# Kernel optimization log

Hardware: AMD Instinct MI355X
Metric: run time of the kernel (lower is better)

## Reference

```python
import jax, jax.numpy as jnp
import numpy as np

N, E, DIN, D, FE, L, B, M = 10000, 40000, 11, 64, 4, 4, 512, 3


def setup_inputs() -> dict:
    key = jax.random.key(0)
    ks = iter(jax.random.split(key, 24))
    s = lambda *sh: jax.random.normal(next(ks), sh, jnp.float32)
    return {
        "x": s(N, DIN),
        "edge_index": jax.random.randint(next(ks), (2, E), 0, N),
        "edge_attr": jax.random.uniform(next(ks), (E, FE), jnp.float32),
        "batch": jnp.sort(jax.random.randint(next(ks), (N,), 0, B)),
        "W0": s(DIN, D) * 0.1, "b0": jnp.zeros((D,), jnp.float32),
        "Wn1": s(FE, 2 * D) * 0.1, "bn1": jnp.zeros((2 * D,), jnp.float32),
        "Wn2": s(2 * D, D * D) * 0.02, "bn2": jnp.zeros((D * D,), jnp.float32),
        "root": s(L, D, D) * 0.1, "conv_bias": jnp.zeros((L, D), jnp.float32),
        "lstm_Wih": s(4 * D, 2 * D) * 0.1, "lstm_Whh": s(4 * D, D) * 0.1,
        "lstm_b": jnp.zeros((4 * D,), jnp.float32),
        "Wo1": s(2 * D, D) * 0.1, "bo1": jnp.zeros((D,), jnp.float32),
        "Wo2": s(D, 1) * 0.1, "bo2": jnp.zeros((1,), jnp.float32),
    }


def reference(x, edge_index, edge_attr, batch, W0, b0, Wn1, bn1, Wn2, bn2,
              root, conv_bias, lstm_Wih, lstm_Whh, lstm_b, Wo1, bo1, Wo2, bo2):
    src, dst = edge_index[0], edge_index[1]
    h = x @ W0 + b0  # [N, D]
    # Edge MLP is SHARED across all conv layers -> compute per-edge weight matrices once
    ew = (jax.nn.silu(edge_attr @ Wn1 + bn1) @ Wn2 + bn2).reshape(E, D, D)
    for l in range(L):
        msg = jnp.einsum('ed,edf->ef', h[src], ew)  # gather-compute per edge
        aggr = jax.ops.segment_sum(msg, dst, num_segments=N)  # scatter-add to targets
        h = h + (aggr + h @ root[l] + conv_bias[l])  # NNConv + residual
    # Set2Set pooling (LSTM, M processing steps)
    q_star = jnp.zeros((B, 2 * D), h.dtype)
    hs = jnp.zeros((B, D), h.dtype)
    cs = jnp.zeros((B, D), h.dtype)
    for _ in range(M):
        gates = q_star @ lstm_Wih.T + hs @ lstm_Whh.T + lstm_b
        i, f, g, o = jnp.split(gates, 4, axis=-1)  # torch LSTM gate order
        cs = jax.nn.sigmoid(f) * cs + jax.nn.sigmoid(i) * jnp.tanh(g)
        hs = jax.nn.sigmoid(o) * jnp.tanh(cs)
        q = hs  # [B, D]
        e = jnp.sum(h * q[batch], axis=-1)  # [N]
        emax = jax.ops.segment_max(e, batch, num_segments=B)
        ex = jnp.exp(e - emax[batch])
        denom = jax.ops.segment_sum(ex, batch, num_segments=B)
        a = ex / denom[batch]  # per-graph softmax attention
        r = jax.ops.segment_sum(a[:, None] * h, batch, num_segments=B)
        q_star = jnp.concatenate([q, r], axis=-1)
    out = jax.nn.silu(q_star @ Wo1 + bo1) @ Wo2 + bo2
    return out.reshape(-1)
```

## Files before the change

kernel.cpp:

```cpp
#include <hip/hip_runtime.h>
#include <cstdint>
#include <cstddef>

#define NN   10000
#define EE   40000
#define DIN_ 11
#define DD   64
#define LL   4
#define BB   512
#define MM   3
#define K1   128
#define DD2  4096
#define NPB  16
#define NCH  8
#define CSPL 2
#define CPB  4
#define ESLOT 12
#define ECREG (8 * ESLOT)
#define EHW (ECREG * 8)

typedef unsigned short ushort_t;
typedef unsigned int   uint_t;

typedef __bf16 bf16x8_t __attribute__((ext_vector_type(8)));
typedef float  f32x4_t  __attribute__((ext_vector_type(4)));
union FragU { uint4 u; bf16x8_t b; };

__device__ __forceinline__ float bfu(ushort_t u) { return __uint_as_float(((uint_t)u) << 16); }
__device__ __forceinline__ float bflo(uint_t u) { return __uint_as_float(u << 16); }
__device__ __forceinline__ float bfhi(uint_t u) { return __uint_as_float(u & 0xffff0000u); }
__device__ __forceinline__ ushort_t f2bf(float f) {
  uint_t u = __float_as_uint(f);
  u = (u + 0x7fffu + ((u >> 16) & 1u)) >> 16;
  return (ushort_t)u;
}
__device__ __forceinline__ uint_t pack2(float lo, float hi) {
  return (uint_t)f2bf(lo) | ((uint_t)f2bf(hi) << 16);
}
__device__ __forceinline__ float sigmf_(float x) { return 1.f / (1.f + expf(-x)); }
__device__ __forceinline__ float siluf_(float x) { return x / (1.f + expf(-x)); }

#if defined(__HIP_DEVICE_COMPILE__) && __has_builtin(__builtin_amdgcn_fdot2_f32_bf16)
typedef __bf16 bf16x2_t __attribute__((ext_vector_type(2)));
__device__ __forceinline__ float dot2a(uint_t a, uint_t b, float c) {
  union { uint_t u; bf16x2_t v; } ua, ub;
  ua.u = a; ub.u = b;
  return __builtin_amdgcn_fdot2_f32_bf16(ua.v, ub.v, c, false);
}
#else
__device__ __forceinline__ float dot2a(uint_t a, uint_t b, float c) {
  return c + bflo(a) * bflo(b) + bfhi(a) * bfhi(b);
}
#endif

#define NCANON 16
struct CanonArgs {
  const void* src[NCANON];
  float* dst[NCANON];
  int n[NCANON];
};
__global__ void k_canon(CanonArgs a, const ushort_t* __restrict__ ea, int* __restrict__ flag) {
  __shared__ int bad;
  if (threadIdx.x == 0) bad = 0;
  __syncthreads();
  ushort_t u = ea[threadIdx.x];
  if ((u & 0x8000u) || u > 0x3F80u) atomicAdd(&bad, 1);
  __syncthreads();
  const int isbf = (bad == 0) ? 1 : 0;
  if (blockIdx.x == 0 && blockIdx.y == 0 && threadIdx.x == 0) *flag = isbf;
  const int ai = blockIdx.y;
  const int n = a.n[ai];
  const int i = blockIdx.x * 256 + threadIdx.x;
  if (i >= n) return;
  float v;
  if (isbf) v = bfu(((const ushort_t*)a.src[ai])[i]);
  else      v = ((const float*)a.src[ai])[i];
  a.dst[ai][i] = v;
}

__global__ void k_wn2m(const void* __restrict__ Wn2, uint_t* __restrict__ out,
                       const int* __restrict__ flag) {
  __shared__ ushort_t row[DD2];
  const int k = blockIdx.x, tid = threadIdx.x;
  if (*flag) {
    const uint4* src = (const uint4*)((const ushort_t*)Wn2 + (size_t)k * DD2);
    ((uint4*)row)[tid] = src[tid];
    ((uint4*)row)[tid + 256] = src[tid + 256];
  } else {
    const float* src = (const float*)Wn2 + (size_t)k * DD2;
    for (int j = 0; j < 16; ++j) row[tid + 256 * j] = f2bf(src[tid + 256 * j]);
  }
  __syncthreads();
  const int kpg = k >> 1, par = k & 1;
  const int lane = tid >> 2, jp = tid & 3;
  const int q = lane >> 4, n = lane & 15;
  for (int fc = 0; fc < 4; ++fc) {
#pragma unroll
    for (int hf = 0; hf < 2; ++hf) {
      int d0 = hf * 32 + q * 8 + 2 * jp;
      int f = fc * 16 + n;
      uint_t lo = row[d0 * 64 + f], hi = row[(d0 + 1) * 64 + f];
      out[((((size_t)kpg * 4 + fc) * 2 + par) * 2 + hf) * 256 + tid] = lo | (hi << 16);
    }
  }
}

__global__ void k_wT(const float* __restrict__ Wihc, const float* __restrict__ Whhc,
                     float* __restrict__ Wiht, float* __restrict__ Whht) {
  int idx = blockIdx.x * 256 + threadIdx.x;
  if (idx < 4 * DD * K1) {
    int j = idx >> 7, i = idx & 127;
    Wiht[i * 256 + j] = Wihc[idx];
  }
  if (idx < 4 * DD * DD) {
    int j = idx >> 6, i = idx & 63;
    Whht[i * 256 + j] = Whhc[idx];
  }
}

__global__ void k_embed(const float* __restrict__ x, const float* __restrict__ W0,
                        const float* __restrict__ b0, const float* __restrict__ bn2,
                        float* __restrict__ h, uint_t* __restrict__ hpk,
                        float* __restrict__ nbias) {
  __shared__ float xs[DIN_];
  __shared__ float hl[DD];
  const int n = blockIdx.x, f = threadIdx.x;
  if (f < DIN_) xs[f] = x[n * DIN_ + f];
  __syncthreads();
  float a = b0[f];
  for (int i = 0; i < DIN_; ++i) a += xs[i] * W0[i * DD + f];
  h[(size_t)n * DD + f] = a;
  hl[f] = a;
  float other = __shfl_down(a, 1);
  if ((f & 1) == 0)
    hpk[(size_t)n * 32 + (f >> 1)] = pack2(a, other);
  __syncthreads();
  float nb = 0.f;
#pragma unroll
  for (int d = 0; d < DD; ++d) nb += hl[d] * bn2[d * DD + f];
  nbias[(size_t)n * DD + f] = nb;
}

__global__ void k_edgemlp(const float* __restrict__ ea, const float* __restrict__ Wn1,
                          const float* __restrict__ bn1, const int* __restrict__ epos,
                          uint_t* __restrict__ hn1c) {
  int idx = blockIdx.x * 256 + threadIdx.x;
  if (idx >= EE * (K1 / 2)) return;
  int e = idx >> 6, j = idx & 63;
  int k0 = 2 * j, k1 = 2 * j + 1;
  float a0 = ea[e * 4 + 0], a1 = ea[e * 4 + 1], a2 = ea[e * 4 + 2], a3 = ea[e * 4 + 3];
  float t0 = bn1[k0] + a0 * Wn1[k0] + a1 * Wn1[K1 + k0] + a2 * Wn1[2 * K1 + k0] + a3 * Wn1[3 * K1 + k0];
  float t1 = bn1[k1] + a0 * Wn1[k1] + a1 * Wn1[K1 + k1] + a2 * Wn1[2 * K1 + k1] + a3 * Wn1[3 * K1 + k1];
  int pos = epos[e];
  hn1c[((size_t)(j >> 3) * EE + pos) * 8 + (j & 7)] = pack2(siluf_(t0), siluf_(t1));
}

__global__ void k_hist(const int* __restrict__ ei, int* __restrict__ cnt_s) {
  int e = blockIdx.x * 256 + threadIdx.x;
  if (e >= EE) return;
  atomicAdd(&cnt_s[ei[e]], 1);
}

__global__ void k_scan(const int* __restrict__ cnt, int* __restrict__ rp,
                       const int* __restrict__ batch, int* __restrict__ goff) {
  if (blockIdx.x == 1) {
    int g = threadIdx.x;
    if (g > BB) return;
    int lo = 0, hi = NN;
    while (lo < hi) {
      int mid = (lo + hi) >> 1;
      if (batch[mid] < g) lo = mid + 1; else hi = mid;
    }
    goff[g] = lo;
    return;
  }
  __shared__ int part[1024];
  const int tid = threadIdx.x;
  const int chunk = (NN + 1023) / 1024;
  int s = 0;
  for (int j = 0; j < chunk; ++j) {
    int idx = tid * chunk + j;
    if (idx < NN) s += cnt[idx];
  }
  part[tid] = s;
  __syncthreads();
  for (int off = 1; off < 1024; off <<= 1) {
    int v = (tid >= off) ? part[tid - off] : 0;
    __syncthreads();
    part[tid] += v;
    __syncthreads();
  }
  int base = (tid == 0) ? 0 : part[tid - 1];
  for (int j = 0; j < chunk; ++j) {
    int idx = tid * chunk + j;
    if (idx < NN) { rp[idx] = base; base += cnt[idx]; }
  }
  if (tid == 1023) rp[NN] = part[1023];
}

__global__ void k_fill(const int* __restrict__ ei, const int* __restrict__ rps,
                       int* __restrict__ cur_s, int* __restrict__ epos,
                       int* __restrict__ esd) {
  int e = blockIdx.x * 256 + threadIdx.x;
  if (e >= EE) return;
  int s = ei[e], d = ei[EE + e];
  int ps = atomicAdd(&cur_s[s], 1);
  int pos = rps[s] + ps;
  epos[e] = pos;
  esd[2 * pos] = s;
  esd[2 * pos + 1] = d;
}

__global__ __launch_bounds__(512, 4) void k_conv(
    const uint_t* __restrict__ hpk, const uint_t* __restrict__ hn1c,
    const uint_t* __restrict__ Wn2m, const float* __restrict__ nbias,
    const int* __restrict__ rps, const int* __restrict__ esd,
    float* __restrict__ aggr) {
  __shared__ __align__(16) uint_t Gp[NPB * 2 * 64 * 4];
  __shared__ __align__(16) uint_t eh[CPB * EHW];
  __shared__ int2 eStage[ECREG];
  const int tid = threadIdx.x;
  const int w = tid >> 6, lane = tid & 63;
  const int q = lane >> 4, n16 = lane & 15;
  const int half = blockIdx.x / 625;
  const int ng = blockIdx.x - half * 625;
  const int n0 = ng * NPB;
  const int e0 = rps[n0], e1 = rps[n0 + NPB];
  const int ecnt = e1 - e0;
  const int ecap = ecnt < ECREG ? ecnt : ECREG;

  if (tid < ECREG && tid < ecnt) eStage[tid] = ((const int2*)esd)[e0 + tid];

  uint4 st0, st1, st2, st3;
  const bool stv = (tid < ecap * 2);
  if (stv) {
    const size_t base = ((size_t)(half * CPB) * EE + e0) * 8;
    st0 = ((const uint4*)(hn1c + base))[tid];
    st1 = ((const uint4*)(hn1c + base + (size_t)EE * 8))[tid];
    st2 = ((const uint4*)(hn1c + base + (size_t)2 * EE * 8))[tid];
    st3 = ((const uint4*)(hn1c + base + (size_t)3 * EE * 8))[tid];
  }

  FragU a0, a1;
  {
    const uint4* ap = (const uint4*)(hpk + (size_t)(n0 + n16) * 32);
    a0.u = ap[q];
    a1.u = ap[4 + q];
  }
  __syncthreads();

  float acc[ESLOT];
#pragma unroll
  for (int s = 0; s < ESLOT; ++s) {
    const int li = w + 8 * s;
    float v = 0.f;
    if (half == 0 && li < ecap)
      v = nbias[(size_t)eStage[li].x * 64 + lane];
    acc[s] = v;
  }

  if (stv) {
    ((uint4*)(eh + 0 * EHW))[tid] = st0;
    ((uint4*)(eh + 1 * EHW))[tid] = st1;
    ((uint4*)(eh + 2 * EHW))[tid] = st2;
    ((uint4*)(eh + 3 * EHW))[tid] = st3;
  }

  const int kq = w >> 2, fcw = w & 3;
  for (int cc = 0; cc < CPB; ++cc) {
    const int c = half * CPB + cc;
    if (cc) __syncthreads();
    uint_t pk[4][4];
#pragma unroll
    for (int slot = 0; slot < 4; ++slot) {
      const int kpg = c * 8 + kq * 4 + slot;
      const uint4* bp = (const uint4*)Wn2m + (size_t)(kpg * 4 + fcw) * 256 + lane;
      FragU b00, b01, b10, b11;
      b00.u = bp[0];
      b01.u = bp[64];
      b10.u = bp[128];
      b11.u = bp[192];
      f32x4_t acc0 = {0.f, 0.f, 0.f, 0.f};
      f32x4_t acc1 = {0.f, 0.f, 0.f, 0.f};
      acc0 = __builtin_amdgcn_mfma_f32_16x16x32_bf16(a0.b, b00.b, acc0, 0, 0, 0);
      acc0 = __builtin_amdgcn_mfma_f32_16x16x32_bf16(a1.b, b01.b, acc0, 0, 0, 0);
      acc1 = __builtin_amdgcn_mfma_f32_16x16x32_bf16(a0.b, b10.b, acc1, 0, 0, 0);
      acc1 = __builtin_amdgcn_mfma_f32_16x16x32_bf16(a1.b, b11.b, acc1, 0, 0, 0);
#pragma unroll
      for (int r = 0; r < 4; ++r) pk[r][slot] = pack2(acc0[r], acc1[r]);
    }
#pragma unroll
    for (int r = 0; r < 4; ++r) {
      const int m = q * 4 + r;
      uint4 v;
      v.x = pk[r][0]; v.y = pk[r][1]; v.z = pk[r][2]; v.w = pk[r][3];
      ((uint4*)Gp)[(size_t)(m * 2 + kq) * 64 + fcw * 16 + n16] = v;
    }
    __syncthreads();
    const uint4* ehb = (const uint4*)(eh + cc * EHW);
#pragma unroll
    for (int s = 0; s < ESLOT; ++s) {
      const int li = w + 8 * s;
      if (li < ecap) {
        const int2 sd = eStage[li];
        const int m = sd.x - n0;
        uint4 hv0 = ehb[li * 2], hv1 = ehb[li * 2 + 1];
        const uint4* gb = (const uint4*)Gp + (size_t)(m * 2) * 64 + lane;
        uint4 g0 = gb[0], g1 = gb[64];
        float p = acc[s];
        p = dot2a(g0.x, hv0.x, p);
        p = dot2a(g0.y, hv0.y, p);
        p = dot2a(g0.z, hv0.z, p);
        p = dot2a(g0.w, hv0.w, p);
        p = dot2a(g1.x, hv1.x, p);
        p = dot2a(g1.y, hv1.y, p);
        p = dot2a(g1.z, hv1.z, p);
        p = dot2a(g1.w, hv1.w, p);
        acc[s] = p;
      }
    }
    for (int li = ECREG + w; li < ecnt; li += 8) {
      const int ii = e0 + li;
      const int src = __builtin_amdgcn_readfirstlane(esd[2 * ii]);
      const int dst = __builtin_amdgcn_readfirstlane(esd[2 * ii + 1]);
      const int m = src - n0;
      float p = (half == 0 && cc == 0) ? nbias[(size_t)src * 64 + lane] : 0.f;
      const uint4* hp = (const uint4*)(hn1c + ((size_t)c * EE + ii) * 8);
      uint4 hv0 = hp[0], hv1 = hp[1];
      const uint4* gb = (const uint4*)Gp + (size_t)(m * 2) * 64 + lane;
      uint4 g0 = gb[0], g1 = gb[64];
      p = dot2a(g0.x, hv0.x, p);
      p = dot2a(g0.y, hv0.y, p);
      p = dot2a(g0.z, hv0.z, p);
      p = dot2a(g0.w, hv0.w, p);
      p = dot2a(g1.x, hv1.x, p);
      p = dot2a(g1.y, hv1.y, p);
      p = dot2a(g1.z, hv1.z, p);
      p = dot2a(g1.w, hv1.w, p);
      atomicAdd(&aggr[(size_t)dst * 64 + lane], p);
    }
  }
#pragma unroll
  for (int s = 0; s < ESLOT; ++s) {
    const int li = w + 8 * s;
    if (li < ecap) {
      const int dst = eStage[li].y;
      atomicAdd(&aggr[(size_t)dst * 64 + lane], acc[s]);
    }
  }
}

__global__ __launch_bounds__(256) void k_update(
    float* __restrict__ h, uint_t* __restrict__ hpk,
    float* __restrict__ aggr, const float* __restrict__ bn2,
    const float* __restrict__ root, const float* __restrict__ cb,
    float* __restrict__ nbias, int l) {
  __shared__ float hl[4][DD];
  __shared__ float al[4][DD];
  const int tid = threadIdx.x, w = tid >> 6, f = tid & 63;
  const int n = blockIdx.x * 4 + w;
  float hv = h[(size_t)n * DD + f];
  hl[w][f] = hv;
  float acc = hv + aggr[(size_t)n * DD + f] + cb[l * DD + f];
  aggr[(size_t)n * DD + f] = 0.f;
  __syncthreads();
  const float* rp = root + (size_t)l * DD2;
#pragma unroll
  for (int d = 0; d < DD; ++d) acc += hl[w][d] * rp[d * DD + f];
  h[(size_t)n * DD + f] = acc;
  al[w][f] = acc;
  float other = __shfl_down(acc, 1);
  if ((f & 1) == 0)
    hpk[(size_t)n * 32 + (f >> 1)] = pack2(acc, other);
  __syncthreads();
  float nb = 0.f;
#pragma unroll
  for (int d = 0; d < DD; ++d) nb += al[w][d] * bn2[d * DD + f];
  nbias[(size_t)n * DD + f] = nb;
}

#define EVCAP 2048
__global__ void k_s2s(const float* __restrict__ h, const int* __restrict__ goff,
                      const float* __restrict__ Wiht, const float* __restrict__ Whht,
                      const float* __restrict__ lb,
                      const float* __restrict__ Wo1, const float* __restrict__ bo1,
                      const float* __restrict__ Wo2, const float* __restrict__ bo2,
                      void* __restrict__ outv, const int* __restrict__ flag) {
  __shared__ float qsl[K1];
  __shared__ float hsl[DD];
  __shared__ float csl[DD];
  __shared__ float gl[4][DD];
  __shared__ float red[256];
  __shared__ float ev[EVCAP];
  __shared__ float rp4[4][DD];
  const int g = blockIdx.x, tid = threadIdx.x;

  if (tid < K1) qsl[tid] = 0.f;
  else if (tid < K1 + DD) hsl[tid - K1] = 0.f;
  else csl[tid - K1 - DD] = 0.f;
  __syncthreads();

  const int i0 = goff[g];
  int cnt = goff[g + 1] - i0;
  if (cnt > EVCAP) cnt = EVCAP;

  for (int m = 0; m < MM; ++m) {
    {
      float a = lb[tid];
      for (int i = 0; i < K1; ++i) a += qsl[i] * Wiht[i * 256 + tid];
      for (int i = 0; i < DD; ++i) a += hsl[i] * Whht[i * 256 + tid];
      gl[tid >> 6][tid & 63] = a;
    }
    __syncthreads();
    if (tid < DD) {
      float ig = sigmf_(gl[0][tid]), fg = sigmf_(gl[1][tid]);
      float gg = tanhf(gl[2][tid]), og = sigmf_(gl[3][tid]);
      float c = fg * csl[tid] + ig * gg;
      csl[tid] = c;
      hsl[tid] = og * tanhf(c);
    }
    __syncthreads();
    float lmax = -1e30f;
    for (int jj = tid; jj < cnt; jj += 256) {
      const float* hp = h + (size_t)(i0 + jj) * DD;
      float e = 0.f;
#pragma unroll
      for (int d = 0; d < DD; ++d) e += hp[d] * hsl[d];
      ev[jj] = e;
      lmax = fmaxf(lmax, e);
    }
    red[tid] = lmax;
    __syncthreads();
    for (int s = 128; s > 0; s >>= 1) {
      if (tid < s) red[tid] = fmaxf(red[tid], red[tid + s]);
      __syncthreads();
    }
    const float emax = red[0];
    __syncthreads();
    float lsum = 0.f;
    for (int jj = tid; jj < cnt; jj += 256) {
      float ex = expf(ev[jj] - emax);
      ev[jj] = ex;
      lsum += ex;
    }
    red[tid] = lsum;
    __syncthreads();
    for (int s = 128; s > 0; s >>= 1) {
      if (tid < s) red[tid] += red[tid + s];
      __syncthreads();
    }
    const float denom = red[0];
    const int f = tid & 63, grp = tid >> 6;
    float acc = 0.f;
    for (int jj = grp; jj < cnt; jj += 4)
      acc += ev[jj] * h[(size_t)(i0 + jj) * DD + f];
    rp4[grp][f] = acc;
    __syncthreads();
    if (tid < DD) {
      float r = rp4[0][tid] + rp4[1][tid] + rp4[2][tid] + rp4[3][tid];
      r = (cnt > 0 && denom > 0.f) ? r / denom : 0.f;
      qsl[tid] = hsl[tid];
      qsl[DD + tid] = r;
    }
    __syncthreads();
  }
  if (tid < DD) {
    float t = bo1[tid];
    for (int i = 0; i < K1; ++i) t += qsl[i] * Wo1[i * DD + tid];
    float s = siluf_(t) * Wo2[tid];
    for (int off = 32; off > 0; off >>= 1) s += __shfl_down(s, off);
    if (tid == 0) {
      float v = s + bo2[0];
      if (*flag) ((ushort_t*)outv)[g] = f2bf(v);
      else       ((float*)outv)[g] = v;
    }
  }
}

extern "C" void kernel_launch(void* const* d_in, const int* in_sizes, int n_in,
                              void* d_out, int out_size, void* d_ws, size_t ws_size,
                              hipStream_t stream) {
  const void* x_r    = d_in[0];
  const int*  ei     = (const int*)d_in[1];
  const void* ea_r   = d_in[2];
  const int*  batch  = (const int*)d_in[3];
  const void* W0_r   = d_in[4];
  const void* b0_r   = d_in[5];
  const void* Wn1_r  = d_in[6];
  const void* bn1_r  = d_in[7];
  const void* Wn2_r  = d_in[8];
  const void* bn2_r  = d_in[9];
  const void* root_r = d_in[10];
  const void* cb_r   = d_in[11];
  const void* Wih_r  = d_in[12];
  const void* Whh_r  = d_in[13];
  const void* lb_r   = d_in[14];
  const void* Wo1_r  = d_in[15];
  const void* bo1_r  = d_in[16];
  const void* Wo2_r  = d_in[17];
  const void* bo2_r  = d_in[18];

  char* w = (char*)d_ws;
  size_t off = 0;
  auto alloc = [&](size_t bytes) -> void* {
    void* p = w + off;
    off = (off + bytes + 255) & ~(size_t)255;
    return p;
  };
  int* flag = (int*)alloc(4);
  float* xc    = (float*)alloc((size_t)NN * DIN_ * 4);
  float* eac   = (float*)alloc((size_t)EE * 4 * 4);
  float* W0c   = (float*)alloc((size_t)DIN_ * DD * 4);
  float* b0c   = (float*)alloc((size_t)DD * 4);
  float* Wn1c  = (float*)alloc((size_t)4 * K1 * 4);
  float* bn1c  = (float*)alloc((size_t)K1 * 4);
  float* bn2c  = (float*)alloc((size_t)DD2 * 4);
  float* rootc = (float*)alloc((size_t)LL * DD2 * 4);
  float* cbc   = (float*)alloc((size_t)LL * DD * 4);
  float* Wihc  = (float*)alloc((size_t)4 * DD * K1 * 4);
  float* Whhc  = (float*)alloc((size_t)4 * DD * DD * 4);
  float* lbc   = (float*)alloc((size_t)4 * DD * 4);
  float* Wo1c  = (float*)alloc((size_t)K1 * DD * 4);
  float* bo1c  = (float*)alloc((size_t)DD * 4);
  float* Wo2c  = (float*)alloc((size_t)DD * 4);
  float* bo2c  = (float*)alloc((size_t)4);
  float* Wiht  = (float*)alloc((size_t)K1 * 256 * 4);
  float* Whht  = (float*)alloc((size_t)DD * 256 * 4);
  uint_t* Wn2m = (uint_t*)alloc((size_t)64 * 4 * 2 * 2 * 64 * 4 * 4);
  float*  h    = (float*)alloc((size_t)NN * DD * 4);
  uint_t* hpk  = (uint_t*)alloc((size_t)NN * 32 * 4);
  uint_t* hn1c = (uint_t*)alloc((size_t)EE * (K1 / 2) * 4);
  float*  aggr = (float*)alloc((size_t)NN * DD * 4);
  float*  nbias= (float*)alloc((size_t)NN * DD * 4);
  int* cnts  = (int*)alloc((size_t)2 * NN * 4);
  int* rps   = (int*)alloc((size_t)(NN + 1) * 4);
  int* epos  = (int*)alloc((size_t)EE * 4);
  int* esd   = (int*)alloc((size_t)2 * EE * 4);
  int* goff  = (int*)alloc((size_t)(BB + 1) * 4);

  int* cnt_s = cnts;
  int* cur_s = cnts + NN;

  hipMemsetAsync(cnts, 0, (size_t)2 * NN * 4, stream);
  hipMemsetAsync(aggr, 0, (size_t)NN * DD * 4, stream);

  CanonArgs ca;
  const void* srcs[NCANON] = {x_r, ea_r, W0_r, b0_r, Wn1_r, bn1_r, bn2_r, root_r,
                              cb_r, Wih_r, Whh_r, lb_r, Wo1_r, bo1_r, Wo2_r, bo2_r};
  float* dsts[NCANON] = {xc, eac, W0c, b0c, Wn1c, bn1c, bn2c, rootc,
                         cbc, Wihc, Whhc, lbc, Wo1c, bo1c, Wo2c, bo2c};
  int cnts_c[NCANON] = {NN * DIN_, EE * 4, DIN_ * DD, DD, 4 * K1, K1, DD2, LL * DD2,
                        LL * DD, 4 * DD * K1, 4 * DD * DD, 4 * DD, K1 * DD, DD, DD, 1};
  for (int i = 0; i < NCANON; ++i) { ca.src[i] = srcs[i]; ca.dst[i] = dsts[i]; ca.n[i] = cnts_c[i]; }
  {
    dim3 grid((EE * 4 + 255) / 256, NCANON);
    k_canon<<<grid, 256, 0, stream>>>(ca, (const ushort_t*)ea_r, flag);
  }
  k_wn2m<<<K1, 256, 0, stream>>>(Wn2_r, Wn2m, flag);
  k_wT<<<(4 * DD * K1 + 255) / 256, 256, 0, stream>>>(Wihc, Whhc, Wiht, Whht);

  k_embed<<<NN, DD, 0, stream>>>(xc, W0c, b0c, bn2c, h, hpk, nbias);
  k_hist<<<(EE + 255) / 256, 256, 0, stream>>>(ei, cnt_s);
  k_scan<<<2, 1024, 0, stream>>>(cnt_s, rps, batch, goff);
  k_fill<<<(EE + 255) / 256, 256, 0, stream>>>(ei, rps, cur_s, epos, esd);
  k_edgemlp<<<(EE * (K1 / 2) + 255) / 256, 256, 0, stream>>>(eac, Wn1c, bn1c, epos, hn1c);

  for (int l = 0; l < LL; ++l) {
    k_conv<<<CSPL * (NN / NPB), 512, 0, stream>>>(hpk, hn1c, Wn2m, nbias, rps, esd, aggr);
    k_update<<<NN / 4, 256, 0, stream>>>(h, hpk, aggr, bn2c, rootc, cbc, nbias, l);
  }

  k_s2s<<<BB, 256, 0, stream>>>(h, goff, Wiht, Whht, lbc, Wo1c, bo1c, Wo2c, bo2c,
                                d_out, flag);
}
```

Measured before the change: 404.5 us.

## Store edge hidden features edge-major and reuse G rows across contiguous edges

Changes the hn1c layout from chunk-major to edge-major (64 packed words per edge), so each conv block loads its edges' half-feature slice with contiguous 16-byte loads into one shared buffer. Edge slots are now assigned contiguously per wave (w*ESLOT+s), so consecutive edges that share a source node can skip reloading the G fragment from LDS. The embedding kernel now packs four nodes per 256-thread block to cut launch and block overhead. The edge-major layout makes the k_edgemlp stores strided differently, and the contiguous slot assignment may unbalance work across waves.

```diff
diff --git a/kernel.cpp b/kernel.cpp
--- a/kernel.cpp
+++ b/kernel.cpp
@@ -17,7 +17,6 @@
 #define CPB  4
 #define ESLOT 12
 #define ECREG (8 * ESLOT)
-#define EHW (ECREG * 8)
 
 typedef unsigned short ushort_t;
 typedef unsigned int   uint_t;
@@ -118,26 +117,28 @@
   }
 }
 
-__global__ void k_embed(const float* __restrict__ x, const float* __restrict__ W0,
-                        const float* __restrict__ b0, const float* __restrict__ bn2,
-                        float* __restrict__ h, uint_t* __restrict__ hpk,
-                        float* __restrict__ nbias) {
-  __shared__ float xs[DIN_];
-  __shared__ float hl[DD];
-  const int n = blockIdx.x, f = threadIdx.x;
-  if (f < DIN_) xs[f] = x[n * DIN_ + f];
+__global__ __launch_bounds__(256) void k_embed(
+    const float* __restrict__ x, const float* __restrict__ W0,
+    const float* __restrict__ b0, const float* __restrict__ bn2,
+    float* __restrict__ h, uint_t* __restrict__ hpk,
+    float* __restrict__ nbias) {
+  __shared__ float xs[4][DIN_];
+  __shared__ float hl[4][DD];
+  const int tid = threadIdx.x, w = tid >> 6, f = tid & 63;
+  const int n = blockIdx.x * 4 + w;
+  if (f < DIN_) xs[w][f] = x[n * DIN_ + f];
   __syncthreads();
   float a = b0[f];
-  for (int i = 0; i < DIN_; ++i) a += xs[i] * W0[i * DD + f];
+  for (int i = 0; i < DIN_; ++i) a += xs[w][i] * W0[i * DD + f];
   h[(size_t)n * DD + f] = a;
-  hl[f] = a;
+  hl[w][f] = a;
   float other = __shfl_down(a, 1);
   if ((f & 1) == 0)
     hpk[(size_t)n * 32 + (f >> 1)] = pack2(a, other);
   __syncthreads();
   float nb = 0.f;
 #pragma unroll
-  for (int d = 0; d < DD; ++d) nb += hl[d] * bn2[d * DD + f];
+  for (int d = 0; d < DD; ++d) nb += hl[w][d] * bn2[d * DD + f];
   nbias[(size_t)n * DD + f] = nb;
 }
 
@@ -152,7 +153,7 @@
   float t0 = bn1[k0] + a0 * Wn1[k0] + a1 * Wn1[K1 + k0] + a2 * Wn1[2 * K1 + k0] + a3 * Wn1[3 * K1 + k0];
   float t1 = bn1[k1] + a0 * Wn1[k1] + a1 * Wn1[K1 + k1] + a2 * Wn1[2 * K1 + k1] + a3 * Wn1[3 * K1 + k1];
   int pos = epos[e];
-  hn1c[((size_t)(j >> 3) * EE + pos) * 8 + (j & 7)] = pack2(siluf_(t0), siluf_(t1));
+  hn1c[(size_t)pos * 64 + j] = pack2(siluf_(t0), siluf_(t1));
 }
 
 __global__ void k_hist(const int* __restrict__ ei, int* __restrict__ cnt_s) {
@@ -217,7 +218,7 @@
     const int* __restrict__ rps, const int* __restrict__ esd,
     float* __restrict__ aggr) {
   __shared__ __align__(16) uint_t Gp[NPB * 2 * 64 * 4];
-  __shared__ __align__(16) uint_t eh[CPB * EHW];
+  __shared__ __align__(16) uint_t eh[ECREG * 32];
   __shared__ int2 eStage[ECREG];
   const int tid = threadIdx.x;
   const int w = tid >> 6, lane = tid & 63;
@@ -231,14 +232,14 @@
 
   if (tid < ECREG && tid < ecnt) eStage[tid] = ((const int2*)esd)[e0 + tid];
 
-  uint4 st0, st1, st2, st3;
-  const bool stv = (tid < ecap * 2);
-  if (stv) {
-    const size_t base = ((size_t)(half * CPB) * EE + e0) * 8;
-    st0 = ((const uint4*)(hn1c + base))[tid];
-    st1 = ((const uint4*)(hn1c + base + (size_t)EE * 8))[tid];
-    st2 = ((const uint4*)(hn1c + base + (size_t)2 * EE * 8))[tid];
-    st3 = ((const uint4*)(hn1c + base + (size_t)3 * EE * 8))[tid];
+  uint4 st0, st1;
+  const bool v0 = (tid < ecap * 8);
+  const bool v1 = (tid + 512 < ecap * 8);
+  if (v0)
+    st0 = *(const uint4*)(hn1c + ((size_t)(e0 + (tid >> 3)) * 64) + half * 32 + (tid & 7) * 4);
+  if (v1) {
+    const int i = tid + 512;
+    st1 = *(const uint4*)(hn1c + ((size_t)(e0 + (i >> 3)) * 64) + half * 32 + (i & 7) * 4);
   }
 
   FragU a0, a1;
@@ -252,19 +253,15 @@
   float acc[ESLOT];
 #pragma unroll
   for (int s = 0; s < ESLOT; ++s) {
-    const int li = w + 8 * s;
+    const int li = w * ESLOT + s;
     float v = 0.f;
     if (half == 0 && li < ecap)
       v = nbias[(size_t)eStage[li].x * 64 + lane];
     acc[s] = v;
   }
 
-  if (stv) {
-    ((uint4*)(eh + 0 * EHW))[tid] = st0;
-    ((uint4*)(eh + 1 * EHW))[tid] = st1;
-    ((uint4*)(eh + 2 * EHW))[tid] = st2;
-    ((uint4*)(eh + 3 * EHW))[tid] = st3;
-  }
+  if (v0) ((uint4*)eh)[tid] = st0;
+  if (v1) ((uint4*)eh)[tid + 512] = st1;
 
   const int kq = w >> 2, fcw = w & 3;
   for (int cc = 0; cc < CPB; ++cc) {
@@ -297,16 +294,22 @@
       ((uint4*)Gp)[(size_t)(m * 2 + kq) * 64 + fcw * 16 + n16] = v;
     }
     __syncthreads();
-    const uint4* ehb = (const uint4*)(eh + cc * EHW);
+    int mPrev = -1;
+    uint4 g0, g1;
 #pragma unroll
     for (int s = 0; s < ESLOT; ++s) {
-      const int li = w + 8 * s;
+      const int li = w * ESLOT + s;
       if (li < ecap) {
         const int2 sd = eStage[li];
         const int m = sd.x - n0;
-        uint4 hv0 = ehb[li * 2], hv1 = ehb[li * 2 + 1];
-        const uint4* gb = (const uint4*)Gp + (size_t)(m * 2) * 64 + lane;
-        uint4 g0 = gb[0], g1 = gb[64];
+        if (m != mPrev) {
+          const uint4* gb = (const uint4*)Gp + (size_t)(m * 2) * 64 + lane;
+          g0 = gb[0];
+          g1 = gb[64];
+          mPrev = m;
+        }
+        const uint_t* ep = eh + li * 32 + cc * 8;
+        uint4 hv0 = ((const uint4*)ep)[0], hv1 = ((const uint4*)ep)[1];
         float p = acc[s];
         p = dot2a(g0.x, hv0.x, p);
         p = dot2a(g0.y, hv0.y, p);
@@ -325,24 +328,24 @@
       const int dst = __builtin_amdgcn_readfirstlane(esd[2 * ii + 1]);
       const int m = src - n0;
       float p = (half == 0 && cc == 0) ? nbias[(size_t)src * 64 + lane] : 0.f;
-      const uint4* hp = (const uint4*)(hn1c + ((size_t)c * EE + ii) * 8);
+      const uint4* hp = (const uint4*)(hn1c + (size_t)ii * 64 + half * 32 + cc * 8);
       uint4 hv0 = hp[0], hv1 = hp[1];
       const uint4* gb = (const uint4*)Gp + (size_t)(m * 2) * 64 + lane;
-      uint4 g0 = gb[0], g1 = gb[64];
-      p = dot2a(g0.x, hv0.x, p);
-      p = dot2a(g0.y, hv0.y, p);
-      p = dot2a(g0.z, hv0.z, p);
-      p = dot2a(g0.w, hv0.w, p);
-      p = dot2a(g1.x, hv1.x, p);
-      p = dot2a(g1.y, hv1.y, p);
-      p = dot2a(g1.z, hv1.z, p);
-      p = dot2a(g1.w, hv1.w, p);
+      uint4 g0o = gb[0], g1o = gb[64];
+      p = dot2a(g0o.x, hv0.x, p);
+      p = dot2a(g0o.y, hv0.y, p);
+      p = dot2a(g0o.z, hv0.z, p);
+      p = dot2a(g0o.w, hv0.w, p);
+      p = dot2a(g1o.x, hv1.x, p);
+      p = dot2a(g1o.y, hv1.y, p);
+      p = dot2a(g1o.z, hv1.z, p);
+      p = dot2a(g1o.w, hv1.w, p);
       atomicAdd(&aggr[(size_t)dst * 64 + lane], p);
     }
   }
 #pragma unroll
   for (int s = 0; s < ESLOT; ++s) {
-    const int li = w + 8 * s;
+    const int li = w * ESLOT + s;
     if (li < ecap) {
       const int dst = eStage[li].y;
       atomicAdd(&aggr[(size_t)dst * 64 + lane], acc[s]);
@@ -559,7 +562,7 @@
   k_wn2m<<<K1, 256, 0, stream>>>(Wn2_r, Wn2m, flag);
   k_wT<<<(4 * DD * K1 + 255) / 256, 256, 0, stream>>>(Wihc, Whhc, Wiht, Whht);
 
-  k_embed<<<NN, DD, 0, stream>>>(xc, W0c, b0c, bn2c, h, hpk, nbias);
+  k_embed<<<NN / 4, 256, 0, stream>>>(xc, W0c, b0c, bn2c, h, hpk, nbias);
   k_hist<<<(EE + 255) / 256, 256, 0, stream>>>(ei, cnt_s);
   k_scan<<<2, 1024, 0, stream>>>(cnt_s, rps, batch, goff);
   k_fill<<<(EE + 255) / 256, 256, 0, stream>>>(ei, rps, cur_s, epos, esd);
```

New measurement: 461.4 us. 1.14x slower.
